# Kernel tuning notes

Hardware: AMD Instinct MI355X
Metric: run time of the kernel (lower is better)

The kernel has to match this reference:

```python
import jax, jax.numpy as jnp
import numpy as np

N_NODES = 100000
N_EDGES = 1600000
N_FEAT = 128
N_HIDDEN = 128
N_CLASS = 64


def setup_inputs() -> dict:
    key = jax.random.key(0)
    ks = jax.random.split(key, 8)
    s = 0.05  # small init scale
    return {
        "x": jax.random.normal(ks[0], (N_NODES, N_FEAT), dtype=jnp.float32),
        "W_l1": jax.random.normal(ks[1], (N_FEAT, N_HIDDEN), dtype=jnp.float32) * s,
        "b_l1": jnp.zeros((N_HIDDEN,), dtype=jnp.float32),
        "W_r1": jax.random.normal(ks[2], (N_FEAT, N_HIDDEN), dtype=jnp.float32) * s,
        "W_l2": jax.random.normal(ks[3], (N_HIDDEN, N_CLASS), dtype=jnp.float32) * s,
        "b_l2": jnp.zeros((N_CLASS,), dtype=jnp.float32),
        "W_r2": jax.random.normal(ks[4], (N_HIDDEN, N_CLASS), dtype=jnp.float32) * s,
        "edge_index": jax.random.randint(ks[5], (2, N_EDGES), 0, N_NODES, dtype=jnp.int64)
        if jax.config.jax_enable_x64 else jax.random.randint(ks[5], (2, N_EDGES), 0, N_NODES, dtype=jnp.int32),
    }


def _sage_conv(h, Wl, bl, Wr, src, dst, n_nodes):
    # PyG SAGEConv, aggr='mean': out = lin_l(mean_j x_j) + lin_r(x_i)
    msg = h[src]                                                 # [E, d] gather
    sums = jax.ops.segment_sum(msg, dst, num_segments=n_nodes)  # [N, d] scatter-add
    cnt = jax.ops.segment_sum(jnp.ones((src.shape[0],), h.dtype), dst,
                              num_segments=n_nodes)             # in-degree
    agg = sums / jnp.maximum(cnt, 1.0)[:, None]                 # mean (0 for isolated)
    return agg @ Wl + bl + h @ Wr


def reference(x, W_l1, b_l1, W_r1, W_l2, b_l2, W_r2, edge_index):
    src, dst = edge_index[0], edge_index[1]
    n = x.shape[0]
    # layer 0: conv -> relu (dropout inactive in eval)
    h = jax.nn.relu(_sage_conv(x, W_l1, b_l1, W_r1, src, dst, n))
    # layer 1 (last, no output_layer): conv only
    return _sage_conv(h, W_l2, b_l2, W_r2, src, dst, n)
```

## Files before the change

### kernel.cpp

```cpp
#include <hip/hip_runtime.h>
#include <cstddef>
#include <cstdint>


#define NC 196
#define CSH 9
#define CCAP 8832
#define FPC 8
#define NPB 64
#define BCAP 1280
#define PAD 56
#define NT1 16
#define NT2 8

typedef __attribute__((ext_vector_type(4))) float f32x4;
typedef __attribute__((ext_vector_type(8))) short bf16x8;

static __device__ __forceinline__ unsigned short f2bf(float f) {
    unsigned u = __float_as_uint(f);
    u += 0x7fffu + ((u >> 16) & 1u);
    return (unsigned short)(u >> 16);
}
static __device__ __forceinline__ float bflo(unsigned u) { return __uint_as_float(u << 16); }
static __device__ __forceinline__ float bfhi(unsigned u) { return __uint_as_float(u & 0xffff0000u); }

__global__ __launch_bounds__(256) void k_prep(
    const float* __restrict__ Wl1, const float* __restrict__ Wr1,
    const float* __restrict__ Wl2, const float* __restrict__ Wr2,
    unsigned short* __restrict__ B1, unsigned short* __restrict__ B2) {
    int gid = blockIdx.x * 256 + threadIdx.x;
    const float* W;
    int col, kb, c;
    unsigned short* dst;
    int stride;
    if (gid < 4096) {
        int ks = gid >> 10, rem = gid & 1023, ct = rem >> 6, l = rem & 63;
        col = ct * 16 + (l & 15);
        kb = ks * 32 + ((l >> 4) << 3);
        W = col < 128 ? Wl1 : Wr1;
        c = col < 128 ? col : col - 128;
        stride = 128;
        dst = B1 + (size_t)gid * 8;
    } else if (gid < 6144) {
        int g2 = gid - 4096;
        int ks = g2 >> 9, rem = g2 & 511, ct = rem >> 6, l = rem & 63;
        col = ct * 16 + (l & 15);
        kb = ks * 32 + ((l >> 4) << 3);
        W = col < 64 ? Wl2 : Wr2;
        c = col < 64 ? col : col - 64;
        stride = 64;
        dst = B2 + (size_t)g2 * 8;
    } else return;
    unsigned v[4];
#pragma unroll
    for (int p = 0; p < 4; p++) {
        unsigned lo = f2bf(W[(size_t)(kb + 2 * p) * stride + c]);
        unsigned hi = f2bf(W[(size_t)(kb + 2 * p + 1) * stride + c]);
        v[p] = lo | (hi << 16);
    }
    *(uint4*)dst = *(uint4*)v;
}

__global__ __launch_bounds__(256) void k_phase1(
    const int* __restrict__ ei, int E,
    const float* __restrict__ x, const unsigned short* __restrict__ B1,
    int* __restrict__ ccnt, unsigned* __restrict__ bktc,
    unsigned short* __restrict__ xl, unsigned short* __restrict__ xr,
    int M, int G_G, int G_B) {
    __shared__ unsigned short Bs[8192];
    __shared__ int cnt[NC], sbase[NC];
    int role = blockIdx.x & 1, idx = blockIdx.x >> 1;
    int tid = threadIdx.x;
    if (role == 1) {
        if (idx >= G_B) return;
        if (tid < NC) cnt[tid] = 0;
        __syncthreads();
        unsigned pk[16];
        int cc[16], rr[16];
        int base_e = idx * 4096;
#pragma unroll
        for (int g = 0; g < 4; g++) {
            int e = base_e + (g * 256 + tid) * 4;
            if (e + 4 <= E) {
                int4 s4 = *(const int4*)(ei + e);
                int4 d4 = *(const int4*)(ei + (size_t)E + e);
                const int* sp = (const int*)&s4;
                const int* dp = (const int*)&d4;
#pragma unroll
                for (int j = 0; j < 4; j++) {
                    int k = g * 4 + j;
                    int dd = dp[j];
                    cc[k] = dd >> CSH;
                    pk[k] = (unsigned)sp[j] | (((unsigned)dd & 511u) << 17);
                    rr[k] = atomicAdd(&cnt[cc[k]], 1);
                }
            } else {
#pragma unroll
                for (int j = 0; j < 4; j++) {
                    int k = g * 4 + j;
                    int ee = e + j;
                    if (ee < E) {
                        int ss = ei[ee], dd = ei[(size_t)E + ee];
                        cc[k] = dd >> CSH;
                        pk[k] = (unsigned)ss | (((unsigned)dd & 511u) << 17);
                        rr[k] = atomicAdd(&cnt[cc[k]], 1);
                    } else cc[k] = -1;
                }
            }
        }
        __syncthreads();
        if (tid < NC) sbase[tid] = atomicAdd(&ccnt[tid], cnt[tid]);
        __syncthreads();
#pragma unroll
        for (int k = 0; k < 16; k++) {
            if (cc[k] >= 0) {
                int pos = sbase[cc[k]] + rr[k];
                if (pos < CCAP) bktc[(size_t)cc[k] * CCAP + pos] = pk[k];
            }
        }
    } else {
        if (idx >= G_G) return;
        int wave = tid >> 6, lane = tid & 63;
        int row0 = idx * 64;
        int xrow = row0 + wave * 16 + (lane & 15);
        int xrc = xrow < M ? xrow : M - 1;
        const float* xp = x + (size_t)xrc * 128 + ((lane >> 4) << 3);
        f32x4 acc[NT1] = {};
        for (int ks = 0; ks < 4; ks++) {
            __syncthreads();
            {
                const uint4* src = (const uint4*)(B1 + (size_t)ks * 8192);
                uint4* dst = (uint4*)Bs;
#pragma unroll
                for (int it = 0; it < 4; it++)
                    dst[it * 256 + tid] = src[it * 256 + tid];
            }
            __syncthreads();
            float4 a0 = *(const float4*)(xp + ks * 32);
            float4 a1 = *(const float4*)(xp + ks * 32 + 4);
            bf16x8 xb;
            xb[0] = (short)f2bf(a0.x); xb[1] = (short)f2bf(a0.y);
            xb[2] = (short)f2bf(a0.z); xb[3] = (short)f2bf(a0.w);
            xb[4] = (short)f2bf(a1.x); xb[5] = (short)f2bf(a1.y);
            xb[6] = (short)f2bf(a1.z); xb[7] = (short)f2bf(a1.w);
#pragma unroll
            for (int ct = 0; ct < NT1; ct++) {
                bf16x8 wf = *(const bf16x8*)&Bs[((ct << 6) + lane) << 3];
                acc[ct] = __builtin_amdgcn_mfma_f32_16x16x32_bf16(
                    wf, xb, acc[ct], 0, 0, 0);
            }
        }
        if (xrow < M) {
#pragma unroll
            for (int ct = 0; ct < NT1; ct++) {
                unsigned short* dstp = (ct < 8) ? xl : xr;
                int colb = (ct & 7) * 16 + ((lane >> 4) << 2);
                ushort4 o;
                o.x = f2bf(acc[ct][0]); o.y = f2bf(acc[ct][1]);
                o.z = f2bf(acc[ct][2]); o.w = f2bf(acc[ct][3]);
                *(ushort4*)(dstp + (size_t)xrow * 128 + colb) = o;
            }
        }
    }
}

__global__ __launch_bounds__(256) void k_refine(
    const int* __restrict__ ccnt, const unsigned* __restrict__ bktc,
    int* __restrict__ bcnt, unsigned* __restrict__ bkt) {
    __shared__ unsigned sorted[CCAP];
    __shared__ int fcnt[FPC], fscan[FPC];
    int b = blockIdx.x, tid = threadIdx.x;
    if (tid < FPC) fcnt[tid] = 0;
    __syncthreads();
    int ne = min(ccnt[b], CCAP);
    const unsigned* seg = bktc + (size_t)b * CCAP;
    for (int i = tid; i < ne; i += 256)
        atomicAdd(&fcnt[(seg[i] >> 17) >> 6], 1);
    __syncthreads();
    if (tid == 0) {
        int s = 0;
        for (int f = 0; f < FPC; f++) { fscan[f] = s; s += fcnt[f]; }
    }
    __syncthreads();
    if (tid < FPC) fcnt[tid] = 0;
    __syncthreads();
    for (int i = tid; i < ne; i += 256) {
        unsigned pk = seg[i];
        int c9 = (int)(pk >> 17);
        int f = c9 >> 6;
        int r = atomicAdd(&fcnt[f], 1);
        sorted[fscan[f] + r] = (pk & 0x1ffffu) | (((unsigned)c9 & 63u) << 17);
    }
    __syncthreads();
#pragma unroll
    for (int f = 0; f < FPC; f++) {
        int fine = b * FPC + f;
        int nf = fcnt[f], off = fscan[f];
        int nfw = nf < BCAP ? nf : BCAP;
        for (int i = tid; i < nfw; i += 256)
            bkt[(size_t)fine * BCAP + i] = sorted[off + i];
        if (tid == 0) bcnt[fine] = nf;
    }
}

__global__ __launch_bounds__(256) void k_aggB(
    const unsigned short* __restrict__ xl, const unsigned short* __restrict__ xr,
    const float* __restrict__ b1,
    const int* __restrict__ bcnt, const unsigned* __restrict__ bkt,
    unsigned short* __restrict__ hb, int n) {
    __shared__ int list[NPB][PAD];
    __shared__ int cnt[NPB];
    int b = blockIdx.x, base = b * NPB, tid = threadIdx.x;
    if (tid < NPB) cnt[tid] = 0;
    __syncthreads();
    int ne = min(bcnt[b], BCAP);
    const unsigned* seg = bkt + (size_t)b * BCAP;
    for (int i = tid; i < ne; i += 256) {
        unsigned pk = seg[i];
        int dl = (int)(pk >> 17);
        int slot = atomicAdd(&cnt[dl], 1);
        if (slot < PAD) list[dl][slot] = (int)(pk & 0x1ffff);
    }
    __syncthreads();
    int lane = tid & 63, wave = tid >> 6;
    const unsigned* xlu = (const unsigned*)xl;
    float2 bb = *(const float2*)(b1 + lane * 2);
    for (int dl = wave; dl < NPB; dl += 4) {
        int node = base + dl;
        if (node >= n) break;
        int c = cnt[dl];
        int m = c < PAD ? c : PAD;
        float a0 = 0.f, a1 = 0.f;
        int e = 0;
        for (; e + 8 <= m; e += 8) {
            int s0 = list[dl][e + 0], s1 = list[dl][e + 1];
            int s2 = list[dl][e + 2], s3 = list[dl][e + 3];
            int s4 = list[dl][e + 4], s5 = list[dl][e + 5];
            int s6 = list[dl][e + 6], s7 = list[dl][e + 7];
            unsigned u0 = xlu[(size_t)s0 * 64 + lane], u1 = xlu[(size_t)s1 * 64 + lane];
            unsigned u2 = xlu[(size_t)s2 * 64 + lane], u3 = xlu[(size_t)s3 * 64 + lane];
            unsigned u4 = xlu[(size_t)s4 * 64 + lane], u5 = xlu[(size_t)s5 * 64 + lane];
            unsigned u6 = xlu[(size_t)s6 * 64 + lane], u7 = xlu[(size_t)s7 * 64 + lane];
            a0 += bflo(u0) + bflo(u1) + bflo(u2) + bflo(u3)
                + bflo(u4) + bflo(u5) + bflo(u6) + bflo(u7);
            a1 += bfhi(u0) + bfhi(u1) + bfhi(u2) + bfhi(u3)
                + bfhi(u4) + bfhi(u5) + bfhi(u6) + bfhi(u7);
        }
        for (; e < m; e++) {
            unsigned u = xlu[(size_t)list[dl][e] * 64 + lane];
            a0 += bflo(u);
            a1 += bfhi(u);
        }
        float inv = c > 0 ? 1.f / (float)c : 0.f;
        unsigned xu = ((const unsigned*)xr)[(size_t)node * 64 + lane];
        float v0 = fmaxf(fmaf(a0, inv, bflo(xu) + bb.x), 0.f);
        float v1 = fmaxf(fmaf(a1, inv, bfhi(xu) + bb.y), 0.f);
        ((unsigned*)hb)[(size_t)node * 64 + lane] =
            (unsigned)f2bf(v0) | ((unsigned)f2bf(v1) << 16);
    }
}

__global__ __launch_bounds__(256) void k_gemm2(
    const unsigned short* __restrict__ hb, const unsigned short* __restrict__ B2,
    unsigned short* __restrict__ hl2, unsigned short* __restrict__ hr2, int M) {
    __shared__ unsigned short Bs[4096];
    int tid = threadIdx.x, wave = tid >> 6, lane = tid & 63;
    int row0 = blockIdx.x * 64;
    int xrow = row0 + wave * 16 + (lane & 15);
    int xrc = xrow < M ? xrow : M - 1;
    const unsigned short* hp = hb + (size_t)xrc * 128 + ((lane >> 4) << 3);
    f32x4 acc[NT2] = {};
    for (int ks = 0; ks < 4; ks++) {
        __syncthreads();
        {
            const uint4* src = (const uint4*)(B2 + (size_t)ks * 4096);
            uint4* dst = (uint4*)Bs;
#pragma unroll
            for (int it = 0; it < 2; it++)
                dst[it * 256 + tid] = src[it * 256 + tid];
        }
        __syncthreads();
        bf16x8 xb = *(const bf16x8*)(hp + ks * 32);
#pragma unroll
        for (int ct = 0; ct < NT2; ct++) {
            bf16x8 wf = *(const bf16x8*)&Bs[((ct << 6) + lane) << 3];
            acc[ct] = __builtin_amdgcn_mfma_f32_16x16x32_bf16(
                wf, xb, acc[ct], 0, 0, 0);
        }
    }
    if (xrow < M) {
#pragma unroll
        for (int ct = 0; ct < NT2; ct++) {
            unsigned short* dstp = (ct < 4) ? hl2 : hr2;
            int colb = (ct & 3) * 16 + ((lane >> 4) << 2);
            ushort4 o;
            o.x = f2bf(acc[ct][0]); o.y = f2bf(acc[ct][1]);
            o.z = f2bf(acc[ct][2]); o.w = f2bf(acc[ct][3]);
            *(ushort4*)(dstp + (size_t)xrow * 64 + colb) = o;
        }
    }
}

__global__ __launch_bounds__(256) void k_aggD(
    const unsigned short* __restrict__ hl2, const unsigned short* __restrict__ hr2,
    const float* __restrict__ b2,
    const int* __restrict__ bcnt, const unsigned* __restrict__ bkt,
    float* __restrict__ out, int n) {
    __shared__ int list[NPB][PAD];
    __shared__ int cnt[NPB];
    int b = blockIdx.x, base = b * NPB, tid = threadIdx.x;
    if (tid < NPB) cnt[tid] = 0;
    __syncthreads();
    int ne = min(bcnt[b], BCAP);
    const unsigned* seg = bkt + (size_t)b * BCAP;
    for (int i = tid; i < ne; i += 256) {
        unsigned pk = seg[i];
        int dl = (int)(pk >> 17);
        int slot = atomicAdd(&cnt[dl], 1);
        if (slot < PAD) list[dl][slot] = (int)(pk & 0x1ffff);
    }
    __syncthreads();
    int l32 = tid & 31, hw = tid >> 5;
    const unsigned* hu = (const unsigned*)hl2;
    float2 bb = *(const float2*)(b2 + l32 * 2);
    for (int dl = hw; dl < NPB; dl += 8) {
        int node = base + dl;
        if (node >= n) break;
        int c = cnt[dl];
        int m = c < PAD ? c : PAD;
        float a0 = 0.f, a1 = 0.f;
        int e = 0;
        for (; e + 8 <= m; e += 8) {
            int s0 = list[dl][e + 0], s1 = list[dl][e + 1];
            int s2 = list[dl][e + 2], s3 = list[dl][e + 3];
            int s4 = list[dl][e + 4], s5 = list[dl][e + 5];
            int s6 = list[dl][e + 6], s7 = list[dl][e + 7];
            unsigned u0 = hu[(size_t)s0 * 32 + l32], u1 = hu[(size_t)s1 * 32 + l32];
            unsigned u2 = hu[(size_t)s2 * 32 + l32], u3 = hu[(size_t)s3 * 32 + l32];
            unsigned u4 = hu[(size_t)s4 * 32 + l32], u5 = hu[(size_t)s5 * 32 + l32];
            unsigned u6 = hu[(size_t)s6 * 32 + l32], u7 = hu[(size_t)s7 * 32 + l32];
            a0 += bflo(u0) + bflo(u1) + bflo(u2) + bflo(u3)
                + bflo(u4) + bflo(u5) + bflo(u6) + bflo(u7);
            a1 += bfhi(u0) + bfhi(u1) + bfhi(u2) + bfhi(u3)
                + bfhi(u4) + bfhi(u5) + bfhi(u6) + bfhi(u7);
        }
        for (; e < m; e++) {
            unsigned u = hu[(size_t)list[dl][e] * 32 + l32];
            a0 += bflo(u);
            a1 += bfhi(u);
        }
        float inv = c > 0 ? 1.f / (float)c : 0.f;
        unsigned ru = ((const unsigned*)hr2)[(size_t)node * 32 + l32];
        float2 o;
        o.x = fmaf(a0, inv, bflo(ru) + bb.x);
        o.y = fmaf(a1, inv, bfhi(ru) + bb.y);
        *(float2*)(out + (size_t)node * 64 + l32 * 2) = o;
    }
}

extern "C" void kernel_launch(void* const* d_in, const int* in_sizes, int n_in,
                              void* d_out, int out_size, void* d_ws, size_t ws_size,
                              hipStream_t stream) {
    const float* x   = (const float*)d_in[0];
    const float* Wl1 = (const float*)d_in[1];
    const float* bl1 = (const float*)d_in[2];
    const float* Wr1 = (const float*)d_in[3];
    const float* Wl2 = (const float*)d_in[4];
    const float* bl2 = (const float*)d_in[5];
    const float* Wr2 = (const float*)d_in[6];
    const int*   ei  = (const int*)d_in[7];
    const int N = in_sizes[0] / 128;
    const int E = in_sizes[7] / 2;
    const int NB = (N + NPB - 1) / NPB;
    const int NBF = NC * FPC;

    auto align = [](size_t v) { return (v + 255) & ~(size_t)255; };
    char* p = (char*)d_ws;
    int* ccnt           = (int*)p;            p += align((size_t)NC * 4);
    unsigned* bktc      = (unsigned*)p;       p += align((size_t)NC * CCAP * 4);
    int* bcnt           = (int*)p;            p += align((size_t)NBF * 4);
    unsigned* bkt       = (unsigned*)p;       p += align((size_t)NBF * BCAP * 4);
    unsigned short* B1  = (unsigned short*)p; p += align((size_t)4096 * 8 * 2);
    unsigned short* B2  = (unsigned short*)p; p += align((size_t)2048 * 8 * 2);
    unsigned short* xl  = (unsigned short*)p; p += align((size_t)N * 128 * 2);
    unsigned short* xr  = (unsigned short*)p; p += align((size_t)N * 128 * 2);
    unsigned short* hb  = (unsigned short*)p; p += align((size_t)N * 128 * 2);
    unsigned short* hl2 = xl;
    unsigned short* hr2 = xl + (size_t)N * 64;

    const int G_G = (N + 63) / 64;
    const int G_B = (E + 4095) / 4096;
    const int G_MAX = G_G > G_B ? G_G : G_B;

    hipMemsetAsync(ccnt, 0, (size_t)NC * 4, stream);
    k_prep<<<24, 256, 0, stream>>>(Wl1, Wr1, Wl2, Wr2, B1, B2);
    k_phase1<<<2 * G_MAX, 256, 0, stream>>>(ei, E, x, B1, ccnt, bktc,
                                            xl, xr, N, G_G, G_B);
    k_refine<<<NC, 256, 0, stream>>>(ccnt, bktc, bcnt, bkt);
    k_aggB<<<NB, 256, 0, stream>>>(xl, xr, bl1, bcnt, bkt, hb, N);
    k_gemm2<<<G_G, 256, 0, stream>>>(hb, B2, hl2, hr2, N);
    k_aggD<<<NB, 256, 0, stream>>>(hl2, hr2, bl2, bcnt, bkt, (float*)d_out, N);
}
```

Baseline: 202.7 us.

## Fuse layer-1 aggregation with second GEMM and read weights directly from global

Merges the layer-1 mean aggregation kernel with the layer-2 projection GEMM. Each block now keeps its 64 hidden rows in shared memory and multiplies them by the layer-2 weights in place, so the hidden activation no longer makes a round trip through global memory and one launch disappears. Both GEMM paths also drop the LDS staging of weight tiles and the barriers around it, reading the small weight matrices straight from global/L2 instead. This relies on the weights staying cache-resident and adds shared-memory use to the aggregation kernel, which may lower its occupancy.

```diff
diff --git a/kernel.cpp b/kernel.cpp
--- a/kernel.cpp
+++ b/kernel.cpp
@@ -67,7 +67,6 @@
     int* __restrict__ ccnt, unsigned* __restrict__ bktc,
     unsigned short* __restrict__ xl, unsigned short* __restrict__ xr,
     int M, int G_G, int G_B) {
-    __shared__ unsigned short Bs[8192];
     __shared__ int cnt[NC], sbase[NC];
     int role = blockIdx.x & 1, idx = blockIdx.x >> 1;
     int tid = threadIdx.x;
@@ -126,16 +125,8 @@
         int xrc = xrow < M ? xrow : M - 1;
         const float* xp = x + (size_t)xrc * 128 + ((lane >> 4) << 3);
         f32x4 acc[NT1] = {};
+#pragma unroll
         for (int ks = 0; ks < 4; ks++) {
-            __syncthreads();
-            {
-                const uint4* src = (const uint4*)(B1 + (size_t)ks * 8192);
-                uint4* dst = (uint4*)Bs;
-#pragma unroll
-                for (int it = 0; it < 4; it++)
-                    dst[it * 256 + tid] = src[it * 256 + tid];
-            }
-            __syncthreads();
             float4 a0 = *(const float4*)(xp + ks * 32);
             float4 a1 = *(const float4*)(xp + ks * 32 + 4);
             bf16x8 xb;
@@ -145,7 +136,7 @@
             xb[6] = (short)f2bf(a1.z); xb[7] = (short)f2bf(a1.w);
 #pragma unroll
             for (int ct = 0; ct < NT1; ct++) {
-                bf16x8 wf = *(const bf16x8*)&Bs[((ct << 6) + lane) << 3];
+                bf16x8 wf = *(const bf16x8*)&B1[((size_t)(ks * 16 + ct) * 64 + lane) * 8];
                 acc[ct] = __builtin_amdgcn_mfma_f32_16x16x32_bf16(
                     wf, xb, acc[ct], 0, 0, 0);
             }
@@ -203,13 +194,14 @@
     }
 }
 
-__global__ __launch_bounds__(256) void k_aggB(
+__global__ __launch_bounds__(256) void k_aggBC(
     const unsigned short* __restrict__ xl, const unsigned short* __restrict__ xr,
-    const float* __restrict__ b1,
+    const float* __restrict__ b1, const unsigned short* __restrict__ B2,
     const int* __restrict__ bcnt, const unsigned* __restrict__ bkt,
-    unsigned short* __restrict__ hb, int n) {
+    unsigned short* __restrict__ hl2, unsigned short* __restrict__ hr2, int n) {
     __shared__ int list[NPB][PAD];
     __shared__ int cnt[NPB];
+    __shared__ unsigned short hs[NPB][136];
     int b = blockIdx.x, base = b * NPB, tid = threadIdx.x;
     if (tid < NPB) cnt[tid] = 0;
     __syncthreads();
@@ -225,70 +217,58 @@
     int lane = tid & 63, wave = tid >> 6;
     const unsigned* xlu = (const unsigned*)xl;
     float2 bb = *(const float2*)(b1 + lane * 2);
-    for (int dl = wave; dl < NPB; dl += 4) {
+#pragma unroll 1
+    for (int it = 0; it < NPB / 4; it++) {
+        int dl = wave + it * 4;
         int node = base + dl;
-        if (node >= n) break;
-        int c = cnt[dl];
-        int m = c < PAD ? c : PAD;
-        float a0 = 0.f, a1 = 0.f;
-        int e = 0;
-        for (; e + 8 <= m; e += 8) {
-            int s0 = list[dl][e + 0], s1 = list[dl][e + 1];
-            int s2 = list[dl][e + 2], s3 = list[dl][e + 3];
-            int s4 = list[dl][e + 4], s5 = list[dl][e + 5];
-            int s6 = list[dl][e + 6], s7 = list[dl][e + 7];
-            unsigned u0 = xlu[(size_t)s0 * 64 + lane], u1 = xlu[(size_t)s1 * 64 + lane];
-            unsigned u2 = xlu[(size_t)s2 * 64 + lane], u3 = xlu[(size_t)s3 * 64 + lane];
-            unsigned u4 = xlu[(size_t)s4 * 64 + lane], u5 = xlu[(size_t)s5 * 64 + lane];
-            unsigned u6 = xlu[(size_t)s6 * 64 + lane], u7 = xlu[(size_t)s7 * 64 + lane];
-            a0 += bflo(u0) + bflo(u1) + bflo(u2) + bflo(u3)
-                + bflo(u4) + bflo(u5) + bflo(u6) + bflo(u7);
-            a1 += bfhi(u0) + bfhi(u1) + bfhi(u2) + bfhi(u3)
-                + bfhi(u4) + bfhi(u5) + bfhi(u6) + bfhi(u7);
-        }
-        for (; e < m; e++) {
-            unsigned u = xlu[(size_t)list[dl][e] * 64 + lane];
-            a0 += bflo(u);
-            a1 += bfhi(u);
-        }
-        float inv = c > 0 ? 1.f / (float)c : 0.f;
-        unsigned xu = ((const unsigned*)xr)[(size_t)node * 64 + lane];
-        float v0 = fmaxf(fmaf(a0, inv, bflo(xu) + bb.x), 0.f);
-        float v1 = fmaxf(fmaf(a1, inv, bfhi(xu) + bb.y), 0.f);
-        ((unsigned*)hb)[(size_t)node * 64 + lane] =
-            (unsigned)f2bf(v0) | ((unsigned)f2bf(v1) << 16);
-    }
-}
-
-__global__ __launch_bounds__(256) void k_gemm2(
-    const unsigned short* __restrict__ hb, const unsigned short* __restrict__ B2,
-    unsigned short* __restrict__ hl2, unsigned short* __restrict__ hr2, int M) {
-    __shared__ unsigned short Bs[4096];
-    int tid = threadIdx.x, wave = tid >> 6, lane = tid & 63;
-    int row0 = blockIdx.x * 64;
-    int xrow = row0 + wave * 16 + (lane & 15);
-    int xrc = xrow < M ? xrow : M - 1;
-    const unsigned short* hp = hb + (size_t)xrc * 128 + ((lane >> 4) << 3);
+        unsigned hv = 0;
+        if (node < n) {
+            int c = cnt[dl];
+            int m = c < PAD ? c : PAD;
+            float a0 = 0.f, a1 = 0.f;
+            int e = 0;
+            for (; e + 8 <= m; e += 8) {
+                int s0 = list[dl][e + 0], s1 = list[dl][e + 1];
+                int s2 = list[dl][e + 2], s3 = list[dl][e + 3];
+                int s4 = list[dl][e + 4], s5 = list[dl][e + 5];
+                int s6 = list[dl][e + 6], s7 = list[dl][e + 7];
+                unsigned u0 = xlu[(size_t)s0 * 64 + lane], u1 = xlu[(size_t)s1 * 64 + lane];
+                unsigned u2 = xlu[(size_t)s2 * 64 + lane], u3 = xlu[(size_t)s3 * 64 + lane];
+                unsigned u4 = xlu[(size_t)s4 * 64 + lane], u5 = xlu[(size_t)s5 * 64 + lane];
+                unsigned u6 = xlu[(size_t)s6 * 64 + lane], u7 = xlu[(size_t)s7 * 64 + lane];
+                a0 += bflo(u0) + bflo(u1) + bflo(u2) + bflo(u3)
+                    + bflo(u4) + bflo(u5) + bflo(u6) + bflo(u7);
+                a1 += bfhi(u0) + bfhi(u1) + bfhi(u2) + bfhi(u3)
+                    + bfhi(u4) + bfhi(u5) + bfhi(u6) + bfhi(u7);
+            }
+            for (; e < m; e++) {
+                unsigned u = xlu[(size_t)list[dl][e] * 64 + lane];
+                a0 += bflo(u);
+                a1 += bfhi(u);
+            }
+            float inv = c > 0 ? 1.f / (float)c : 0.f;
+            unsigned xu = ((const unsigned*)xr)[(size_t)node * 64 + lane];
+            float v0 = fmaxf(fmaf(a0, inv, bflo(xu) + bb.x), 0.f);
+            float v1 = fmaxf(fmaf(a1, inv, bfhi(xu) + bb.y), 0.f);
+            hv = (unsigned)f2bf(v0) | ((unsigned)f2bf(v1) << 16);
+        }
+        *(unsigned*)&hs[dl][lane * 2] = hv;
+    }
+    __syncthreads();
+    int lrow = wave * 16 + (lane & 15);
+    int xrow = base + lrow;
     f32x4 acc[NT2] = {};
+#pragma unroll
     for (int ks = 0; ks < 4; ks++) {
-        __syncthreads();
-        {
-            const uint4* src = (const uint4*)(B2 + (size_t)ks * 4096);
-            uint4* dst = (uint4*)Bs;
-#pragma unroll
-            for (int it = 0; it < 2; it++)
-                dst[it * 256 + tid] = src[it * 256 + tid];
-        }
-        __syncthreads();
-        bf16x8 xb = *(const bf16x8*)(hp + ks * 32);
+        bf16x8 xb = *(const bf16x8*)&hs[lrow][((lane >> 4) << 3) + ks * 32];
 #pragma unroll
         for (int ct = 0; ct < NT2; ct++) {
-            bf16x8 wf = *(const bf16x8*)&Bs[((ct << 6) + lane) << 3];
+            bf16x8 wf = *(const bf16x8*)&B2[((size_t)(ks * 8 + ct) * 64 + lane) * 8];
             acc[ct] = __builtin_amdgcn_mfma_f32_16x16x32_bf16(
                 wf, xb, acc[ct], 0, 0, 0);
         }
     }
-    if (xrow < M) {
+    if (xrow < n) {
 #pragma unroll
         for (int ct = 0; ct < NT2; ct++) {
             unsigned short* dstp = (ct < 4) ? hl2 : hr2;
@@ -384,9 +364,9 @@
     unsigned short* B2  = (unsigned short*)p; p += align((size_t)2048 * 8 * 2);
     unsigned short* xl  = (unsigned short*)p; p += align((size_t)N * 128 * 2);
     unsigned short* xr  = (unsigned short*)p; p += align((size_t)N * 128 * 2);
-    unsigned short* hb  = (unsigned short*)p; p += align((size_t)N * 128 * 2);
-    unsigned short* hl2 = xl;
-    unsigned short* hr2 = xl + (size_t)N * 64;
+    unsigned short* hx  = (unsigned short*)p; p += align((size_t)N * 128 * 2);
+    unsigned short* hl2 = hx;
+    unsigned short* hr2 = hx + (size_t)N * 64;
 
     const int G_G = (N + 63) / 64;
     const int G_B = (E + 4095) / 4096;
@@ -397,7 +377,6 @@
     k_phase1<<<2 * G_MAX, 256, 0, stream>>>(ei, E, x, B1, ccnt, bktc,
                                             xl, xr, N, G_G, G_B);
     k_refine<<<NC, 256, 0, stream>>>(ccnt, bktc, bcnt, bkt);
-    k_aggB<<<NB, 256, 0, stream>>>(xl, xr, bl1, bcnt, bkt, hb, N);
-    k_gemm2<<<G_G, 256, 0, stream>>>(hb, B2, hl2, hr2, N);
+    k_aggBC<<<NB, 256, 0, stream>>>(xl, xr, bl1, B2, bcnt, bkt, hl2, hr2, N);
     k_aggD<<<NB, 256, 0, stream>>>(hl2, hr2, bl2, bcnt, bkt, (float*)d_out, N);
 }
```

New measurement: 238.3 us. 17.6% more time.

## Build CSR per coarse bucket in-place and aggregate directly from it

Applied to the files above, without the earlier changes.

Replaces the two-level refine into fine buckets, and the per-block LDS list build done in both aggregation kernels, with a single counting sort per coarse bucket. That sort writes destination-sorted sources in place plus per-node degree and row offset. The aggregation kernels then assign one wave (or half-wave) per node and read neighbor indices straight from the CSR segment, removing the duplicated LDS bucketing and the PAD truncation. The cost is per-edge index loads from global memory, which are uniform within a wave, and a larger-LDS sort kernel.

```diff
diff --git a/kernel.cpp b/kernel.cpp
--- a/kernel.cpp
+++ b/kernel.cpp
@@ -5,11 +5,8 @@
 
 #define NC 196
 #define CSH 9
+#define CNODES 512
 #define CCAP 8832
-#define FPC 8
-#define NPB 64
-#define BCAP 1280
-#define PAD 56
 #define NT1 16
 #define NT2 8
 
@@ -164,100 +161,96 @@
     }
 }
 
-__global__ __launch_bounds__(256) void k_refine(
-    const int* __restrict__ ccnt, const unsigned* __restrict__ bktc,
-    int* __restrict__ bcnt, unsigned* __restrict__ bkt) {
-    __shared__ unsigned sorted[CCAP];
-    __shared__ int fcnt[FPC], fscan[FPC];
+__global__ __launch_bounds__(256) void k_sort(
+    const int* __restrict__ ccnt, unsigned* __restrict__ bktc,
+    int* __restrict__ deg, int* __restrict__ rowb, int n) {
+    __shared__ unsigned buf[CCAP];
+    __shared__ unsigned short rank[CCAP];
+    __shared__ int cnt[CNODES];
+    __shared__ int base[CNODES];
+    __shared__ int wsum[4];
     int b = blockIdx.x, tid = threadIdx.x;
-    if (tid < FPC) fcnt[tid] = 0;
+    for (int i = tid; i < CNODES; i += 256) cnt[i] = 0;
     __syncthreads();
     int ne = min(ccnt[b], CCAP);
-    const unsigned* seg = bktc + (size_t)b * CCAP;
-    for (int i = tid; i < ne; i += 256)
-        atomicAdd(&fcnt[(seg[i] >> 17) >> 6], 1);
+    unsigned* seg = bktc + (size_t)b * CCAP;
+    for (int i = tid; i < ne; i += 256) {
+        unsigned pk = seg[i];
+        buf[i] = pk;
+        rank[i] = (unsigned short)atomicAdd(&cnt[pk >> 17], 1);
+    }
     __syncthreads();
-    if (tid == 0) {
-        int s = 0;
-        for (int f = 0; f < FPC; f++) { fscan[f] = s; s += fcnt[f]; }
-    }
-    __syncthreads();
-    if (tid < FPC) fcnt[tid] = 0;
+    {
+        int v0 = cnt[2 * tid], v1 = cnt[2 * tid + 1], v = v0 + v1;
+        int lane = tid & 63, wid = tid >> 6;
+        int sv = v;
+#pragma unroll
+        for (int d = 1; d < 64; d <<= 1) {
+            int t = __shfl_up(sv, d);
+            if (lane >= d) sv += t;
+        }
+        if (lane == 63) wsum[wid] = sv;
+        __syncthreads();
+        int wb = 0;
+#pragma unroll
+        for (int w = 0; w < 4; w++) if (w < wid) wb += wsum[w];
+        int ex = wb + sv - v;
+        base[2 * tid] = ex;
+        base[2 * tid + 1] = ex + v0;
+    }
     __syncthreads();
     for (int i = tid; i < ne; i += 256) {
-        unsigned pk = seg[i];
-        int c9 = (int)(pk >> 17);
-        int f = c9 >> 6;
-        int r = atomicAdd(&fcnt[f], 1);
-        sorted[fscan[f] + r] = (pk & 0x1ffffu) | (((unsigned)c9 & 63u) << 17);
-    }
-    __syncthreads();
-#pragma unroll
-    for (int f = 0; f < FPC; f++) {
-        int fine = b * FPC + f;
-        int nf = fcnt[f], off = fscan[f];
-        int nfw = nf < BCAP ? nf : BCAP;
-        for (int i = tid; i < nfw; i += 256)
-            bkt[(size_t)fine * BCAP + i] = sorted[off + i];
-        if (tid == 0) bcnt[fine] = nf;
+        unsigned pk = buf[i];
+        int dl = (int)(pk >> 17);
+        seg[base[dl] + rank[i]] = pk & 0x1ffffu;
+    }
+    for (int dl = tid; dl < CNODES; dl += 256) {
+        int node = (b << CSH) + dl;
+        if (node < n) {
+            deg[node] = cnt[dl];
+            rowb[node] = b * CCAP + base[dl];
+        }
     }
 }
 
 __global__ __launch_bounds__(256) void k_aggB(
     const unsigned short* __restrict__ xl, const unsigned short* __restrict__ xr,
     const float* __restrict__ b1,
-    const int* __restrict__ bcnt, const unsigned* __restrict__ bkt,
+    const int* __restrict__ deg, const int* __restrict__ rowb,
+    const unsigned* __restrict__ sorted,
     unsigned short* __restrict__ hb, int n) {
-    __shared__ int list[NPB][PAD];
-    __shared__ int cnt[NPB];
-    int b = blockIdx.x, base = b * NPB, tid = threadIdx.x;
-    if (tid < NPB) cnt[tid] = 0;
-    __syncthreads();
-    int ne = min(bcnt[b], BCAP);
-    const unsigned* seg = bkt + (size_t)b * BCAP;
-    for (int i = tid; i < ne; i += 256) {
-        unsigned pk = seg[i];
-        int dl = (int)(pk >> 17);
-        int slot = atomicAdd(&cnt[dl], 1);
-        if (slot < PAD) list[dl][slot] = (int)(pk & 0x1ffff);
-    }
-    __syncthreads();
-    int lane = tid & 63, wave = tid >> 6;
+    int gw = (int)((blockIdx.x * 256u + threadIdx.x) >> 6);
+    int lane = threadIdx.x & 63;
+    if (gw >= n) return;
+    int c = deg[gw];
+    const unsigned* seg = sorted + rowb[gw];
     const unsigned* xlu = (const unsigned*)xl;
+    float a0 = 0.f, a1 = 0.f;
+    int e = 0;
+    for (; e + 8 <= c; e += 8) {
+        unsigned s0 = seg[e + 0], s1 = seg[e + 1], s2 = seg[e + 2], s3 = seg[e + 3];
+        unsigned s4 = seg[e + 4], s5 = seg[e + 5], s6 = seg[e + 6], s7 = seg[e + 7];
+        unsigned u0 = xlu[(size_t)s0 * 64 + lane], u1 = xlu[(size_t)s1 * 64 + lane];
+        unsigned u2 = xlu[(size_t)s2 * 64 + lane], u3 = xlu[(size_t)s3 * 64 + lane];
+        unsigned u4 = xlu[(size_t)s4 * 64 + lane], u5 = xlu[(size_t)s5 * 64 + lane];
+        unsigned u6 = xlu[(size_t)s6 * 64 + lane], u7 = xlu[(size_t)s7 * 64 + lane];
+        a0 += bflo(u0) + bflo(u1) + bflo(u2) + bflo(u3)
+            + bflo(u4) + bflo(u5) + bflo(u6) + bflo(u7);
+        a1 += bfhi(u0) + bfhi(u1) + bfhi(u2) + bfhi(u3)
+            + bfhi(u4) + bfhi(u5) + bfhi(u6) + bfhi(u7);
+    }
+    for (; e < c; e++) {
+        unsigned u = xlu[(size_t)seg[e] * 64 + lane];
+        a0 += bflo(u);
+        a1 += bfhi(u);
+    }
+    float inv = (c > 0) ? 1.0f / (float)c : 0.f;
     float2 bb = *(const float2*)(b1 + lane * 2);
-    for (int dl = wave; dl < NPB; dl += 4) {
-        int node = base + dl;
-        if (node >= n) break;
-        int c = cnt[dl];
-        int m = c < PAD ? c : PAD;
-        float a0 = 0.f, a1 = 0.f;
-        int e = 0;
-        for (; e + 8 <= m; e += 8) {
-            int s0 = list[dl][e + 0], s1 = list[dl][e + 1];
-            int s2 = list[dl][e + 2], s3 = list[dl][e + 3];
-            int s4 = list[dl][e + 4], s5 = list[dl][e + 5];
-            int s6 = list[dl][e + 6], s7 = list[dl][e + 7];
-            unsigned u0 = xlu[(size_t)s0 * 64 + lane], u1 = xlu[(size_t)s1 * 64 + lane];
-            unsigned u2 = xlu[(size_t)s2 * 64 + lane], u3 = xlu[(size_t)s3 * 64 + lane];
-            unsigned u4 = xlu[(size_t)s4 * 64 + lane], u5 = xlu[(size_t)s5 * 64 + lane];
-            unsigned u6 = xlu[(size_t)s6 * 64 + lane], u7 = xlu[(size_t)s7 * 64 + lane];
-            a0 += bflo(u0) + bflo(u1) + bflo(u2) + bflo(u3)
-                + bflo(u4) + bflo(u5) + bflo(u6) + bflo(u7);
-            a1 += bfhi(u0) + bfhi(u1) + bfhi(u2) + bfhi(u3)
-                + bfhi(u4) + bfhi(u5) + bfhi(u6) + bfhi(u7);
-        }
-        for (; e < m; e++) {
-            unsigned u = xlu[(size_t)list[dl][e] * 64 + lane];
-            a0 += bflo(u);
-            a1 += bfhi(u);
-        }
-        float inv = c > 0 ? 1.f / (float)c : 0.f;
-        unsigned xu = ((const unsigned*)xr)[(size_t)node * 64 + lane];
-        float v0 = fmaxf(fmaf(a0, inv, bflo(xu) + bb.x), 0.f);
-        float v1 = fmaxf(fmaf(a1, inv, bfhi(xu) + bb.y), 0.f);
-        ((unsigned*)hb)[(size_t)node * 64 + lane] =
-            (unsigned)f2bf(v0) | ((unsigned)f2bf(v1) << 16);
-    }
+    unsigned xu = ((const unsigned*)xr)[(size_t)gw * 64 + lane];
+    float v0 = fmaxf(fmaf(a0, inv, bflo(xu) + bb.x), 0.f);
+    float v1 = fmaxf(fmaf(a1, inv, bfhi(xu) + bb.y), 0.f);
+    ((unsigned*)hb)[(size_t)gw * 64 + lane] =
+        (unsigned)f2bf(v0) | ((unsigned)f2bf(v1) << 16);
 }
 
 __global__ __launch_bounds__(256) void k_gemm2(
@@ -304,58 +297,41 @@
 __global__ __launch_bounds__(256) void k_aggD(
     const unsigned short* __restrict__ hl2, const unsigned short* __restrict__ hr2,
     const float* __restrict__ b2,
-    const int* __restrict__ bcnt, const unsigned* __restrict__ bkt,
+    const int* __restrict__ deg, const int* __restrict__ rowb,
+    const unsigned* __restrict__ sorted,
     float* __restrict__ out, int n) {
-    __shared__ int list[NPB][PAD];
-    __shared__ int cnt[NPB];
-    int b = blockIdx.x, base = b * NPB, tid = threadIdx.x;
-    if (tid < NPB) cnt[tid] = 0;
-    __syncthreads();
-    int ne = min(bcnt[b], BCAP);
-    const unsigned* seg = bkt + (size_t)b * BCAP;
-    for (int i = tid; i < ne; i += 256) {
-        unsigned pk = seg[i];
-        int dl = (int)(pk >> 17);
-        int slot = atomicAdd(&cnt[dl], 1);
-        if (slot < PAD) list[dl][slot] = (int)(pk & 0x1ffff);
-    }
-    __syncthreads();
-    int l32 = tid & 31, hw = tid >> 5;
+    int hw = (int)((blockIdx.x * 256u + threadIdx.x) >> 5);
+    int l32 = threadIdx.x & 31;
+    if (hw >= n) return;
+    int c = deg[hw];
+    const unsigned* seg = sorted + rowb[hw];
     const unsigned* hu = (const unsigned*)hl2;
+    float a0 = 0.f, a1 = 0.f;
+    int e = 0;
+    for (; e + 8 <= c; e += 8) {
+        unsigned s0 = seg[e + 0], s1 = seg[e + 1], s2 = seg[e + 2], s3 = seg[e + 3];
+        unsigned s4 = seg[e + 4], s5 = seg[e + 5], s6 = seg[e + 6], s7 = seg[e + 7];
+        unsigned u0 = hu[(size_t)s0 * 32 + l32], u1 = hu[(size_t)s1 * 32 + l32];
+        unsigned u2 = hu[(size_t)s2 * 32 + l32], u3 = hu[(size_t)s3 * 32 + l32];
+        unsigned u4 = hu[(size_t)s4 * 32 + l32], u5 = hu[(size_t)s5 * 32 + l32];
+        unsigned u6 = hu[(size_t)s6 * 32 + l32], u7 = hu[(size_t)s7 * 32 + l32];
+        a0 += bflo(u0) + bflo(u1) + bflo(u2) + bflo(u3)
+            + bflo(u4) + bflo(u5) + bflo(u6) + bflo(u7);
+        a1 += bfhi(u0) + bfhi(u1) + bfhi(u2) + bfhi(u3)
+            + bfhi(u4) + bfhi(u5) + bfhi(u6) + bfhi(u7);
+    }
+    for (; e < c; e++) {
+        unsigned u = hu[(size_t)seg[e] * 32 + l32];
+        a0 += bflo(u);
+        a1 += bfhi(u);
+    }
+    float inv = (c > 0) ? 1.0f / (float)c : 0.f;
     float2 bb = *(const float2*)(b2 + l32 * 2);
-    for (int dl = hw; dl < NPB; dl += 8) {
-        int node = base + dl;
-        if (node >= n) break;
-        int c = cnt[dl];
-        int m = c < PAD ? c : PAD;
-        float a0 = 0.f, a1 = 0.f;
-        int e = 0;
-        for (; e + 8 <= m; e += 8) {
-            int s0 = list[dl][e + 0], s1 = list[dl][e + 1];
-            int s2 = list[dl][e + 2], s3 = list[dl][e + 3];
-            int s4 = list[dl][e + 4], s5 = list[dl][e + 5];
-            int s6 = list[dl][e + 6], s7 = list[dl][e + 7];
-            unsigned u0 = hu[(size_t)s0 * 32 + l32], u1 = hu[(size_t)s1 * 32 + l32];
-            unsigned u2 = hu[(size_t)s2 * 32 + l32], u3 = hu[(size_t)s3 * 32 + l32];
-            unsigned u4 = hu[(size_t)s4 * 32 + l32], u5 = hu[(size_t)s5 * 32 + l32];
-            unsigned u6 = hu[(size_t)s6 * 32 + l32], u7 = hu[(size_t)s7 * 32 + l32];
-            a0 += bflo(u0) + bflo(u1) + bflo(u2) + bflo(u3)
-                + bflo(u4) + bflo(u5) + bflo(u6) + bflo(u7);
-            a1 += bfhi(u0) + bfhi(u1) + bfhi(u2) + bfhi(u3)
-                + bfhi(u4) + bfhi(u5) + bfhi(u6) + bfhi(u7);
-        }
-        for (; e < m; e++) {
-            unsigned u = hu[(size_t)list[dl][e] * 32 + l32];
-            a0 += bflo(u);
-            a1 += bfhi(u);
-        }
-        float inv = c > 0 ? 1.f / (float)c : 0.f;
-        unsigned ru = ((const unsigned*)hr2)[(size_t)node * 32 + l32];
-        float2 o;
-        o.x = fmaf(a0, inv, bflo(ru) + bb.x);
-        o.y = fmaf(a1, inv, bfhi(ru) + bb.y);
-        *(float2*)(out + (size_t)node * 64 + l32 * 2) = o;
-    }
+    unsigned ru = ((const unsigned*)hr2)[(size_t)hw * 32 + l32];
+    float2 o;
+    o.x = fmaf(a0, inv, bflo(ru) + bb.x);
+    o.y = fmaf(a1, inv, bfhi(ru) + bb.y);
+    *(float2*)(out + (size_t)hw * 64 + l32 * 2) = o;
 }
 
 extern "C" void kernel_launch(void* const* d_in, const int* in_sizes, int n_in,
@@ -371,15 +347,13 @@
     const int*   ei  = (const int*)d_in[7];
     const int N = in_sizes[0] / 128;
     const int E = in_sizes[7] / 2;
-    const int NB = (N + NPB - 1) / NPB;
-    const int NBF = NC * FPC;
 
     auto align = [](size_t v) { return (v + 255) & ~(size_t)255; };
     char* p = (char*)d_ws;
     int* ccnt           = (int*)p;            p += align((size_t)NC * 4);
     unsigned* bktc      = (unsigned*)p;       p += align((size_t)NC * CCAP * 4);
-    int* bcnt           = (int*)p;            p += align((size_t)NBF * 4);
-    unsigned* bkt       = (unsigned*)p;       p += align((size_t)NBF * BCAP * 4);
+    int* deg            = (int*)p;            p += align((size_t)N * 4);
+    int* rowb           = (int*)p;            p += align((size_t)N * 4);
     unsigned short* B1  = (unsigned short*)p; p += align((size_t)4096 * 8 * 2);
     unsigned short* B2  = (unsigned short*)p; p += align((size_t)2048 * 8 * 2);
     unsigned short* xl  = (unsigned short*)p; p += align((size_t)N * 128 * 2);
@@ -396,8 +370,10 @@
     k_prep<<<24, 256, 0, stream>>>(Wl1, Wr1, Wl2, Wr2, B1, B2);
     k_phase1<<<2 * G_MAX, 256, 0, stream>>>(ei, E, x, B1, ccnt, bktc,
                                             xl, xr, N, G_G, G_B);
-    k_refine<<<NC, 256, 0, stream>>>(ccnt, bktc, bcnt, bkt);
-    k_aggB<<<NB, 256, 0, stream>>>(xl, xr, bl1, bcnt, bkt, hb, N);
+    k_sort<<<NC, 256, 0, stream>>>(ccnt, bktc, deg, rowb, N);
+    k_aggB<<<(N * 64 + 255) / 256, 256, 0, stream>>>(xl, xr, bl1, deg, rowb,
+                                                     bktc, hb, N);
     k_gemm2<<<G_G, 256, 0, stream>>>(hb, B2, hl2, hr2, N);
-    k_aggD<<<NB, 256, 0, stream>>>(hl2, hr2, bl2, bcnt, bkt, (float*)d_out, N);
-}
+    k_aggD<<<(N * 32 + 255) / 256, 256, 0, stream>>>(hl2, hr2, bl2, deg, rowb,
+                                                     bktc, (float*)d_out, N);
+}
```

Result: slower. 218.7 us (+7.9%).
